# Kernel optimization log

Hardware: AMD Instinct MI355X
Metric: run time of the kernel (lower is better)

## Reference

```python
import jax, jax.numpy as jnp
import numpy as np

N_NODES = 50000
N_EDGES = 800000
NODE_DIM = 256
HIDDEN_DIM = 256
LN_EPS = 1e-5


def setup_inputs() -> dict:
    key = jax.random.key(0)
    ks = jax.random.split(key, 8)
    d, h = NODE_DIM, HIDDEN_DIM
    return {
        "node_features": jax.random.normal(ks[0], (N_NODES, d), jnp.float32),
        "src": jax.random.randint(ks[1], (N_EDGES,), 0, N_NODES, jnp.int32),
        "dst": jax.random.randint(ks[2], (N_EDGES,), 0, N_NODES, jnp.int32),
        "edge_weight": jax.random.uniform(ks[3], (N_EDGES,), jnp.float32),
        "W1": jax.random.normal(ks[4], (d, h), jnp.float32) / np.sqrt(d),
        "b1": jnp.zeros((h,), jnp.float32),
        "g1": jnp.ones((h,), jnp.float32),
        "be1": jnp.zeros((h,), jnp.float32),
        "W2": jax.random.normal(ks[5], (h, h), jnp.float32) / np.sqrt(h),
        "b2": jnp.zeros((h,), jnp.float32),
        "g2": jnp.ones((h,), jnp.float32),
        "be2": jnp.zeros((h,), jnp.float32),
        "Wp": jax.random.normal(ks[6], (h, d), jnp.float32) / np.sqrt(h),
        "bp": jnp.zeros((d,), jnp.float32),
    }


def _spmm(src, dst, w, x, n):
    # sparse adj @ x : agg[i] = sum_{edges e with dst=i} w_e * x[src_e]
    return jax.ops.segment_sum(w[:, None] * x[src], dst, num_segments=n)


def _layer_norm(x, g, b):
    mu = jnp.mean(x, -1, keepdims=True)
    var = jnp.mean(jnp.square(x - mu), -1, keepdims=True)
    return (x - mu) * jax.lax.rsqrt(var + LN_EPS) * g + b


def reference(node_features, src, dst, edge_weight, W1, b1, g1, be1, W2, b2, g2, be2, Wp, bp):
    n = node_features.shape[0]
    x = node_features
    for (W, b, g, be) in ((W1, b1, g1, be1), (W2, b2, g2, be2)):
        agg = _spmm(src, dst, edge_weight, x, n)
        h = (x + agg) @ W + b
        x = jax.nn.gelu(_layer_norm(h, g, be), approximate=False)
        # Dropout(0.1) is identity in eval mode
    return x @ Wp + bp
```

## Files before the change

### kernel.cpp

```cpp
#include <hip/hip_runtime.h>
#include <hip/hip_bf16.h>
#include <math.h>

#define N_NODES 50000
#define N_EDGES 800000
#define DIM 256
#define MPAD 50176
#define LN_EPS 1e-5f
#define SCAN_BLOCKS 196

typedef short bf16x8 __attribute__((ext_vector_type(8)));
typedef float f32x16 __attribute__((ext_vector_type(16)));
typedef unsigned short u16;
typedef u16 u16x8 __attribute__((ext_vector_type(8)));

__device__ __forceinline__ u16 f2bf(float f) {
    union { float f; unsigned u; } v; v.f = f;
    unsigned r = (v.u + 0x7FFFu + ((v.u >> 16) & 1u)) >> 16;
    return (u16)r;
}
__device__ __forceinline__ float bf2f(u16 h) {
    union { unsigned u; float f; } v; v.u = ((unsigned)h) << 16;
    return v.f;
}
__device__ __forceinline__ float gelu_f(float x) {
    float z = x * (1.595769122f + 0.0713548162726f * x * x);
    return x * (1.0f / (1.0f + __expf(-z)));
}

__global__ void count_kernel(const int* __restrict__ dst, int* __restrict__ counts) {
    int e = blockIdx.x * 256 + threadIdx.x;
    if (e < N_EDGES) atomicAdd(&counts[dst[e]], 1);
}

__global__ void scan1_kernel(const int* __restrict__ counts, int* __restrict__ offsets,
                             int* __restrict__ bsum) {
    __shared__ int sh[256];
    int t = threadIdx.x;
    int idx = blockIdx.x * 256 + t;
    int v = (idx < N_NODES) ? counts[idx] : 0;
    sh[t] = v;
    __syncthreads();
#pragma unroll
    for (int off = 1; off < 256; off <<= 1) {
        int u = (t >= off) ? sh[t - off] : 0;
        __syncthreads();
        sh[t] += u;
        __syncthreads();
    }
    if (idx < N_NODES) offsets[idx] = sh[t] - v;
    if (t == 255) bsum[blockIdx.x] = sh[255];
}

__global__ void scan2_kernel(const int* __restrict__ bsum, int* __restrict__ bbase) {
    __shared__ int sh[256];
    int t = threadIdx.x;
    int v = (t < SCAN_BLOCKS) ? bsum[t] : 0;
    sh[t] = v;
    __syncthreads();
#pragma unroll
    for (int off = 1; off < 256; off <<= 1) {
        int u = (t >= off) ? sh[t - off] : 0;
        __syncthreads();
        sh[t] += u;
        __syncthreads();
    }
    if (t < SCAN_BLOCKS) bbase[t] = sh[t] - v;
}

__global__ void scan3_kernel(int* __restrict__ offsets, const int* __restrict__ bbase,
                             int* __restrict__ cursor) {
    int idx = blockIdx.x * 256 + threadIdx.x;
    if (idx < N_NODES) {
        int o = offsets[idx] + bbase[blockIdx.x];
        offsets[idx] = o;
        cursor[idx] = o;
    }
    if (idx == 0) offsets[N_NODES] = N_EDGES;
}

__global__ void scatter_kernel(const int* __restrict__ src, const int* __restrict__ dst,
                               const float* __restrict__ w, int* __restrict__ cursor,
                               int2* __restrict__ ep) {
    int e = blockIdx.x * 256 + threadIdx.x;
    if (e < N_EDGES) {
        int d = dst[e];
        int p = atomicAdd(&cursor[d], 1);
        int2 v; v.x = src[e]; v.y = __float_as_int(w[e]);
        ep[p] = v;
    }
}

__global__ void conv_kernel(const float* __restrict__ in, u16* __restrict__ out) {
    int i = blockIdx.x * 256 + threadIdx.x;
    float4 v = ((const float4*)in)[i];
    ushort4 o;
    o.x = f2bf(v.x); o.y = f2bf(v.y); o.z = f2bf(v.z); o.w = f2bf(v.w);
    ((ushort4*)out)[i] = o;
}

__global__ void convw_kernel(const float* __restrict__ W1, const float* __restrict__ W2,
                             const float* __restrict__ Wp, u16* __restrict__ BF) {
    int idx = blockIdx.x * 256 + threadIdx.x;
    int j = idx & 7;
    int lane = (idx >> 3) & 63;
    int kb = (idx >> 9) & 15;
    int t = (idx >> 13) & 7;
    int m = idx >> 16;
    int n = t * 32 + (lane & 31);
    int k = kb * 16 + (lane >> 5) * 8 + j;
    const float* W = (m == 0) ? W1 : (m == 1) ? W2 : Wp;
    BF[idx] = f2bf(W[k * 256 + n]);
}

__global__ __launch_bounds__(256) void spmm_kernel(
        const u16* __restrict__ x, const int* __restrict__ offs,
        const int2* __restrict__ ep, u16* __restrict__ y) {
    __shared__ u16 tile[32 * 264];
    int tid = threadIdx.x;
    int wave = tid >> 6;
    int lane = tid & 63;
    int node0 = blockIdx.x * 32 + wave * 8;

    const ushort4* xv = (const ushort4*)x;
#pragma unroll 1
    for (int i = 0; i < 8; ++i) {
        int node = node0 + i;
        float a0 = 0, a1 = 0, a2 = 0, a3 = 0;
        float b0 = 0, b1 = 0, b2 = 0, b3 = 0;
        float c0 = 0, c1 = 0, c2 = 0, c3 = 0;
        float d0 = 0, d1 = 0, d2 = 0, d3 = 0;
        if (node < N_NODES) {
            ushort4 v = xv[(size_t)node * 64 + lane];
            a0 = bf2f(v.x); a1 = bf2f(v.y); a2 = bf2f(v.z); a3 = bf2f(v.w);
            int p = offs[node];
            int p1 = offs[node + 1];
            for (; p + 4 <= p1; p += 4) {
                int2 e0 = ep[p],     e1 = ep[p + 1];
                int2 e2 = ep[p + 2], e3 = ep[p + 3];
                int s0 = e0.x; float w0 = __int_as_float(e0.y);
                int s1 = e1.x; float w1 = __int_as_float(e1.y);
                int s2 = e2.x; float w2 = __int_as_float(e2.y);
                int s3 = e3.x; float w3 = __int_as_float(e3.y);
                ushort4 v0 = xv[(size_t)s0 * 64 + lane];
                ushort4 v1 = xv[(size_t)s1 * 64 + lane];
                ushort4 v2 = xv[(size_t)s2 * 64 + lane];
                ushort4 v3 = xv[(size_t)s3 * 64 + lane];
                a0 += w0 * bf2f(v0.x); a1 += w0 * bf2f(v0.y); a2 += w0 * bf2f(v0.z); a3 += w0 * bf2f(v0.w);
                b0 += w1 * bf2f(v1.x); b1 += w1 * bf2f(v1.y); b2 += w1 * bf2f(v1.z); b3 += w1 * bf2f(v1.w);
                c0 += w2 * bf2f(v2.x); c1 += w2 * bf2f(v2.y); c2 += w2 * bf2f(v2.z); c3 += w2 * bf2f(v2.w);
                d0 += w3 * bf2f(v3.x); d1 += w3 * bf2f(v3.y); d2 += w3 * bf2f(v3.z); d3 += w3 * bf2f(v3.w);
            }
            for (; p < p1; ++p) {
                int2 e = ep[p];
                int s = e.x;
                float w = __int_as_float(e.y);
                ushort4 vv = xv[(size_t)s * 64 + lane];
                a0 += w * bf2f(vv.x); a1 += w * bf2f(vv.y); a2 += w * bf2f(vv.z); a3 += w * bf2f(vv.w);
            }
            a0 += b0 + c0 + d0; a1 += b1 + c1 + d1;
            a2 += b2 + c2 + d2; a3 += b3 + c3 + d3;
        }
        ushort4 o;
        o.x = f2bf(a0); o.y = f2bf(a1); o.z = f2bf(a2); o.w = f2bf(a3);
        ((ushort4*)&tile[(wave * 8 + i) * 264])[lane] = o;
    }
    __syncthreads();
    u16* outb = y + (size_t)blockIdx.x * 8192;
#pragma unroll
    for (int hh = 0; hh < 4; ++hh) {
        int gi = tid + hh * 256;
        int kb = gi >> 6;
        int rem = gi & 63;
        int hf = rem >> 5, m = rem & 31;
        u16x8 v = *(const u16x8*)&tile[m * 264 + kb * 16 + hf * 8];
        *(u16x8*)(outb + (size_t)gi * 8) = v;
    }
}

template <int MODE, int OUT_TILED>
__global__ __launch_bounds__(256, 2) void gemm_kernel(
        const u16* __restrict__ A, const u16* __restrict__ BF,
        const float* __restrict__ bias, const float* __restrict__ g,
        const float* __restrict__ be, u16* __restrict__ xb_out,
        float* __restrict__ f_out) {
    int tid = threadIdx.x;
    int wave = tid >> 6, lane = tid & 63;
    int l31 = lane & 31, half = lane >> 5;

    int tile = blockIdx.x * 4 + wave;
    const u16* ga = A + (size_t)tile * 8192 + lane * 8;
    const u16* gb = BF + lane * 8;
    bf16x8 p = *(const bf16x8*)ga;

    f32x16 acc[8];
#pragma unroll
    for (int t = 0; t < 8; ++t)
#pragma unroll
        for (int r = 0; r < 16; ++r) acc[t][r] = 0.f;

#pragma unroll
    for (int kb = 0; kb < 16; ++kb) {
        bf16x8 a = p;
        if (kb < 15) p = *(const bf16x8*)(ga + (kb + 1) * 512);
#pragma unroll
        for (int t = 0; t < 8; ++t) {
            bf16x8 bf = *(const bf16x8*)(gb + (size_t)(t * 16 + kb) * 512);
            acc[t] = __builtin_amdgcn_mfma_f32_32x32x16_bf16(a, bf, acc[t], 0, 0, 0);
        }
    }

    float bv[8];
#pragma unroll
    for (int t = 0; t < 8; ++t) bv[t] = bias[t * 32 + l31];

    if (MODE == 0) {
        float gv[8], bev[8];
#pragma unroll
        for (int t = 0; t < 8; ++t) {
            int c = t * 32 + l31;
            gv[t] = g[c]; bev[t] = be[c];
        }
#pragma unroll
        for (int r = 0; r < 16; ++r) {
            float s = 0.f, q = 0.f;
#pragma unroll
            for (int t = 0; t < 8; ++t) {
                float v = acc[t][r] + bv[t];
                acc[t][r] = v;
                s += v; q += v * v;
            }
            for (int off = 1; off < 32; off <<= 1) {
                s += __shfl_xor(s, off);
                q += __shfl_xor(q, off);
            }
            float mu = s * (1.0f / 256.0f);
            float var = q * (1.0f / 256.0f) - mu * mu;
            float rs = rsqrtf(var + LN_EPS);
            int m = (r & 3) + 8 * (r >> 2) + 4 * half;
            int row = tile * 32 + m;
#pragma unroll
            for (int t = 0; t < 8; ++t) {
                int c = t * 32 + l31;
                float v = (acc[t][r] - mu) * rs * gv[t] + bev[t];
                u16 ob = f2bf(gelu_f(v));
                if (OUT_TILED) {
                    size_t o = (size_t)tile * 8192 +
                               ((size_t)(c >> 4) * 64 + ((c >> 3) & 1) * 32 + m) * 8 + (c & 7);
                    xb_out[o] = ob;
                } else {
                    xb_out[(size_t)row * 256 + c] = ob;
                }
            }
        }
    } else {
#pragma unroll
        for (int r = 0; r < 16; ++r) {
            int m = (r & 3) + 8 * (r >> 2) + 4 * half;
            int row = tile * 32 + m;
            if (row < N_NODES) {
#pragma unroll
                for (int t = 0; t < 8; ++t) {
                    int c = t * 32 + l31;
                    f_out[(size_t)row * 256 + c] = acc[t][r] + bv[t];
                }
            }
        }
    }
}

extern "C" void kernel_launch(void* const* d_in, const int* in_sizes, int n_in,
                              void* d_out, int out_size, void* d_ws, size_t ws_size,
                              hipStream_t stream) {
    const float* nodef = (const float*)d_in[0];
    const int*   src   = (const int*)d_in[1];
    const int*   dst   = (const int*)d_in[2];
    const float* ew    = (const float*)d_in[3];
    const float* W1 = (const float*)d_in[4];
    const float* b1 = (const float*)d_in[5];
    const float* g1 = (const float*)d_in[6];
    const float* be1 = (const float*)d_in[7];
    const float* W2 = (const float*)d_in[8];
    const float* b2 = (const float*)d_in[9];
    const float* g2 = (const float*)d_in[10];
    const float* be2 = (const float*)d_in[11];
    const float* Wp = (const float*)d_in[12];
    const float* bp = (const float*)d_in[13];
    float* out = (float*)d_out;

    char* ws = (char*)d_ws;
    size_t off = 0;
    auto alloc = [&](size_t bytes) -> void* {
        void* p = ws + off;
        off += (bytes + 255) & ~(size_t)255;
        return p;
    };
    u16*   ybuf    = (u16*)alloc((size_t)MPAD * 256 * 2);
    u16*   xbuf    = (u16*)alloc((size_t)MPAD * 256 * 2);
    u16*   WT      = (u16*)alloc((size_t)3 * 65536 * 2);
    int*   counts  = (int*)alloc((size_t)N_NODES * 4);
    int*   offsets = (int*)alloc((size_t)(N_NODES + 1) * 4);
    int*   cursor  = (int*)alloc((size_t)N_NODES * 4);
    int2*  ep      = (int2*)alloc((size_t)N_EDGES * 8);
    int*   bsum    = (int*)alloc((size_t)SCAN_BLOCKS * 4);
    int*   bbase   = (int*)alloc((size_t)SCAN_BLOCKS * 4);

    hipMemsetAsync(counts, 0, (size_t)N_NODES * 4, stream);
    count_kernel<<<(N_EDGES + 255) / 256, 256, 0, stream>>>(dst, counts);
    scan1_kernel<<<SCAN_BLOCKS, 256, 0, stream>>>(counts, offsets, bsum);
    scan2_kernel<<<1, 256, 0, stream>>>(bsum, bbase);
    scan3_kernel<<<SCAN_BLOCKS, 256, 0, stream>>>(offsets, bbase, cursor);
    scatter_kernel<<<(N_EDGES + 255) / 256, 256, 0, stream>>>(src, dst, ew, cursor, ep);
    conv_kernel<<<N_NODES * 64 / 256, 256, 0, stream>>>(nodef, xbuf);
    convw_kernel<<<768, 256, 0, stream>>>(W1, W2, Wp, WT);

    const int GB = MPAD / 128;
    const int SB = MPAD / 32;
    spmm_kernel<<<SB, 256, 0, stream>>>(xbuf, offsets, ep, ybuf);
    gemm_kernel<0, 0><<<GB, 256, 0, stream>>>(ybuf, WT, b1, g1, be1, xbuf, nullptr);
    spmm_kernel<<<SB, 256, 0, stream>>>(xbuf, offsets, ep, ybuf);
    gemm_kernel<0, 1><<<GB, 256, 0, stream>>>(ybuf, WT + 65536, b2, g2, be2, ybuf, nullptr);
    gemm_kernel<1, 0><<<GB, 256, 0, stream>>>(ybuf, WT + 2 * 65536, bp, nullptr, nullptr, nullptr, out);
}
```

Baseline: 443.0 us.

## Fuse SpMM aggregation with GEMM, LayerNorm and GELU per layer

Merges each layer's SpMM kernel and the following GEMM+LayerNorm+GELU kernel into one kernel. The aggregated 32-row tile stays in shared memory and feeds MFMA directly, and each wave computes two 32-column output tiles. LayerNorm statistics are reduced across waves through shared memory. This removes the global write and re-read of the intermediate bf16 tile and two kernel launches. In exchange, every block re-reads the full weight matrix from global/L2 and adds block-wide syncs.

```diff
diff --git a/kernel.cpp b/kernel.cpp
--- a/kernel.cpp
+++ b/kernel.cpp
@@ -113,13 +113,19 @@
     BF[idx] = f2bf(W[k * 256 + n]);
 }
 
-__global__ __launch_bounds__(256) void spmm_kernel(
+template <int OUT_TILED>
+__global__ __launch_bounds__(256, 4) void fused_kernel(
         const u16* __restrict__ x, const int* __restrict__ offs,
-        const int2* __restrict__ ep, u16* __restrict__ y) {
+        const int2* __restrict__ ep, const u16* __restrict__ BF,
+        const float* __restrict__ bias, const float* __restrict__ g,
+        const float* __restrict__ be, u16* __restrict__ out) {
     __shared__ u16 tile[32 * 264];
+    __shared__ float red[32][8];
+    __shared__ float mur[32], rsr[32];
     int tid = threadIdx.x;
     int wave = tid >> 6;
     int lane = tid & 63;
+    int l31 = lane & 31, half = lane >> 5;
     int node0 = blockIdx.x * 32 + wave * 8;
 
     const ushort4* xv = (const ushort4*)x;
@@ -166,31 +172,81 @@
         ((ushort4*)&tile[(wave * 8 + i) * 264])[lane] = o;
     }
     __syncthreads();
-    u16* outb = y + (size_t)blockIdx.x * 8192;
-#pragma unroll
-    for (int hh = 0; hh < 4; ++hh) {
-        int gi = tid + hh * 256;
-        int kb = gi >> 6;
-        int rem = gi & 63;
-        int hf = rem >> 5, m = rem & 31;
-        u16x8 v = *(const u16x8*)&tile[m * 264 + kb * 16 + hf * 8];
-        *(u16x8*)(outb + (size_t)gi * 8) = v;
-    }
-}
-
-template <int MODE, int OUT_TILED>
-__global__ __launch_bounds__(256, 2) void gemm_kernel(
+
+    int t0 = wave * 2, t1 = wave * 2 + 1;
+    const u16* gb = BF + (size_t)lane * 8;
+    f32x16 acc0, acc1;
+#pragma unroll
+    for (int r = 0; r < 16; ++r) { acc0[r] = 0.f; acc1[r] = 0.f; }
+#pragma unroll
+    for (int kb = 0; kb < 16; ++kb) {
+        bf16x8 a = *(const bf16x8*)&tile[l31 * 264 + kb * 16 + half * 8];
+        bf16x8 bf0 = *(const bf16x8*)(gb + (size_t)(t0 * 16 + kb) * 512);
+        bf16x8 bf1 = *(const bf16x8*)(gb + (size_t)(t1 * 16 + kb) * 512);
+        acc0 = __builtin_amdgcn_mfma_f32_32x32x16_bf16(a, bf0, acc0, 0, 0, 0);
+        acc1 = __builtin_amdgcn_mfma_f32_32x32x16_bf16(a, bf1, acc1, 0, 0, 0);
+    }
+
+    float bv0 = bias[t0 * 32 + l31], bv1 = bias[t1 * 32 + l31];
+    float gv0 = g[t0 * 32 + l31],    gv1 = g[t1 * 32 + l31];
+    float ev0 = be[t0 * 32 + l31],   ev1 = be[t1 * 32 + l31];
+#pragma unroll
+    for (int r = 0; r < 16; ++r) {
+        float v0 = acc0[r] + bv0, v1 = acc1[r] + bv1;
+        acc0[r] = v0; acc1[r] = v1;
+        float s = v0 + v1, q = v0 * v0 + v1 * v1;
+#pragma unroll
+        for (int off = 1; off < 32; off <<= 1) {
+            s += __shfl_xor(s, off);
+            q += __shfl_xor(q, off);
+        }
+        if (l31 == 0) {
+            int rw = (r & 3) + 8 * (r >> 2) + 4 * half;
+            red[rw][wave * 2] = s;
+            red[rw][wave * 2 + 1] = q;
+        }
+    }
+    __syncthreads();
+    if (tid < 32) {
+        float s = red[tid][0] + red[tid][2] + red[tid][4] + red[tid][6];
+        float q = red[tid][1] + red[tid][3] + red[tid][5] + red[tid][7];
+        float mu = s * (1.0f / 256.0f);
+        float var = q * (1.0f / 256.0f) - mu * mu;
+        mur[tid] = mu;
+        rsr[tid] = rsqrtf(var + LN_EPS);
+    }
+    __syncthreads();
+#pragma unroll
+    for (int r = 0; r < 16; ++r) {
+        int rw = (r & 3) + 8 * (r >> 2) + 4 * half;
+        float mu = mur[rw], rs = rsr[rw];
+        float v0 = (acc0[r] - mu) * rs * gv0 + ev0;
+        float v1 = (acc1[r] - mu) * rs * gv1 + ev1;
+        u16 o0 = f2bf(gelu_f(v0));
+        u16 o1 = f2bf(gelu_f(v1));
+        int c0 = t0 * 32 + l31, c1 = t1 * 32 + l31;
+        if (OUT_TILED) {
+            size_t base = (size_t)blockIdx.x * 8192;
+            out[base + ((size_t)(c0 >> 4) * 64 + ((c0 >> 3) & 1) * 32 + rw) * 8 + (c0 & 7)] = o0;
+            out[base + ((size_t)(c1 >> 4) * 64 + ((c1 >> 3) & 1) * 32 + rw) * 8 + (c1 & 7)] = o1;
+        } else {
+            size_t rg = (size_t)(blockIdx.x * 32 + rw) * 256;
+            out[rg + c0] = o0;
+            out[rg + c1] = o1;
+        }
+    }
+}
+
+__global__ __launch_bounds__(256, 2) void proj_kernel(
         const u16* __restrict__ A, const u16* __restrict__ BF,
-        const float* __restrict__ bias, const float* __restrict__ g,
-        const float* __restrict__ be, u16* __restrict__ xb_out,
-        float* __restrict__ f_out) {
+        const float* __restrict__ bias, float* __restrict__ f_out) {
     int tid = threadIdx.x;
     int wave = tid >> 6, lane = tid & 63;
     int l31 = lane & 31, half = lane >> 5;
 
     int tile = blockIdx.x * 4 + wave;
     const u16* ga = A + (size_t)tile * 8192 + lane * 8;
-    const u16* gb = BF + lane * 8;
+    const u16* gb = BF + (size_t)lane * 8;
     bf16x8 p = *(const bf16x8*)ga;
 
     f32x16 acc[8];
@@ -214,56 +270,15 @@
 #pragma unroll
     for (int t = 0; t < 8; ++t) bv[t] = bias[t * 32 + l31];
 
-    if (MODE == 0) {
-        float gv[8], bev[8];
-#pragma unroll
-        for (int t = 0; t < 8; ++t) {
-            int c = t * 32 + l31;
-            gv[t] = g[c]; bev[t] = be[c];
-        }
-#pragma unroll
-        for (int r = 0; r < 16; ++r) {
-            float s = 0.f, q = 0.f;
-#pragma unroll
-            for (int t = 0; t < 8; ++t) {
-                float v = acc[t][r] + bv[t];
-                acc[t][r] = v;
-                s += v; q += v * v;
-            }
-            for (int off = 1; off < 32; off <<= 1) {
-                s += __shfl_xor(s, off);
-                q += __shfl_xor(q, off);
-            }
-            float mu = s * (1.0f / 256.0f);
-            float var = q * (1.0f / 256.0f) - mu * mu;
-            float rs = rsqrtf(var + LN_EPS);
-            int m = (r & 3) + 8 * (r >> 2) + 4 * half;
-            int row = tile * 32 + m;
+#pragma unroll
+    for (int r = 0; r < 16; ++r) {
+        int m = (r & 3) + 8 * (r >> 2) + 4 * half;
+        int row = tile * 32 + m;
+        if (row < N_NODES) {
 #pragma unroll
             for (int t = 0; t < 8; ++t) {
                 int c = t * 32 + l31;
-                float v = (acc[t][r] - mu) * rs * gv[t] + bev[t];
-                u16 ob = f2bf(gelu_f(v));
-                if (OUT_TILED) {
-                    size_t o = (size_t)tile * 8192 +
-                               ((size_t)(c >> 4) * 64 + ((c >> 3) & 1) * 32 + m) * 8 + (c & 7);
-                    xb_out[o] = ob;
-                } else {
-                    xb_out[(size_t)row * 256 + c] = ob;
-                }
-            }
-        }
-    } else {
-#pragma unroll
-        for (int r = 0; r < 16; ++r) {
-            int m = (r & 3) + 8 * (r >> 2) + 4 * half;
-            int row = tile * 32 + m;
-            if (row < N_NODES) {
-#pragma unroll
-                for (int t = 0; t < 8; ++t) {
-                    int c = t * 32 + l31;
-                    f_out[(size_t)row * 256 + c] = acc[t][r] + bv[t];
-                }
+                f_out[(size_t)row * 256 + c] = acc[t][r] + bv[t];
             }
         }
     }
@@ -314,11 +329,9 @@
     conv_kernel<<<N_NODES * 64 / 256, 256, 0, stream>>>(nodef, xbuf);
     convw_kernel<<<768, 256, 0, stream>>>(W1, W2, Wp, WT);
 
+    const int SB = MPAD / 32;
     const int GB = MPAD / 128;
-    const int SB = MPAD / 32;
-    spmm_kernel<<<SB, 256, 0, stream>>>(xbuf, offsets, ep, ybuf);
-    gemm_kernel<0, 0><<<GB, 256, 0, stream>>>(ybuf, WT, b1, g1, be1, xbuf, nullptr);
-    spmm_kernel<<<SB, 256, 0, stream>>>(xbuf, offsets, ep, ybuf);
-    gemm_kernel<0, 1><<<GB, 256, 0, stream>>>(ybuf, WT + 65536, b2, g2, be2, ybuf, nullptr);
-    gemm_kernel<1, 0><<<GB, 256, 0, stream>>>(ybuf, WT + 2 * 65536, bp, nullptr, nullptr, nullptr, out);
-}
+    fused_kernel<0><<<SB, 256, 0, stream>>>(xbuf, offsets, ep, WT, b1, g1, be1, ybuf);
+    fused_kernel<1><<<SB, 256, 0, stream>>>(ybuf, offsets, ep, WT + 65536, b2, g2, be2, xbuf);
+    proj_kernel<<<GB, 256, 0, stream>>>(xbuf, WT + 2 * 65536, bp, out);
+}
```

New measurement: 438.3 us. Within noise of the previous version (-1.1%).

## Split SpMM gather into column slices with edge-parallel lane groups

Applied to the files above, without the earlier changes.

Replaces the SpMM kernel with a column-sliced gather. Each block handles one 32-column slice of a 32-node tile, so the grid grows eightfold. Within a wave, four 16-lane groups work on different edges in parallel and are combined with cross-lane shuffles. Each slice also writes straight into the GEMM's tiled layout. The intent is to shrink the per-node gathered row footprint so it fits in cache better and to raise parallelism; the cost is 64-byte row segments per gather, re-reading the edge list once per slice, and more blocks. It also changes which buffer the second GEMM writes and the third GEMM reads.

```diff
diff --git a/kernel.cpp b/kernel.cpp
--- a/kernel.cpp
+++ b/kernel.cpp
@@ -13,6 +13,7 @@
 typedef float f32x16 __attribute__((ext_vector_type(16)));
 typedef unsigned short u16;
 typedef u16 u16x8 __attribute__((ext_vector_type(8)));
+typedef unsigned int u32;
 
 __device__ __forceinline__ u16 f2bf(float f) {
     union { float f; unsigned u; } v; v.f = f;
@@ -113,69 +114,51 @@
     BF[idx] = f2bf(W[k * 256 + n]);
 }
 
-__global__ __launch_bounds__(256) void spmm_kernel(
+__global__ __launch_bounds__(256) void cgather_kernel(
         const u16* __restrict__ x, const int* __restrict__ offs,
         const int2* __restrict__ ep, u16* __restrict__ y) {
-    __shared__ u16 tile[32 * 264];
+    __shared__ __align__(16) u16 stg[1024];
+    int bid = blockIdx.x;
+    int slice = bid & 7;
+    int tile = bid >> 3;
     int tid = threadIdx.x;
-    int wave = tid >> 6;
-    int lane = tid & 63;
-    int node0 = blockIdx.x * 32 + wave * 8;
-
-    const ushort4* xv = (const ushort4*)x;
+    int wave = tid >> 6, lane = tid & 63;
+    int grp = lane >> 4;
+    int l16 = lane & 15;
+    const u16* xs = x + slice * 32;
+
 #pragma unroll 1
     for (int i = 0; i < 8; ++i) {
-        int node = node0 + i;
-        float a0 = 0, a1 = 0, a2 = 0, a3 = 0;
-        float b0 = 0, b1 = 0, b2 = 0, b3 = 0;
-        float c0 = 0, c1 = 0, c2 = 0, c3 = 0;
-        float d0 = 0, d1 = 0, d2 = 0, d3 = 0;
+        int node = tile * 32 + wave * 8 + i;
+        float a0 = 0.f, a1 = 0.f;
         if (node < N_NODES) {
-            ushort4 v = xv[(size_t)node * 64 + lane];
-            a0 = bf2f(v.x); a1 = bf2f(v.y); a2 = bf2f(v.z); a3 = bf2f(v.w);
-            int p = offs[node];
+            if (grp == 0) {
+                u32 sv = *(const u32*)(xs + (size_t)node * 256 + l16 * 2);
+                a0 = __uint_as_float(sv << 16);
+                a1 = __uint_as_float(sv & 0xffff0000u);
+            }
             int p1 = offs[node + 1];
-            for (; p + 4 <= p1; p += 4) {
-                int2 e0 = ep[p],     e1 = ep[p + 1];
-                int2 e2 = ep[p + 2], e3 = ep[p + 3];
-                int s0 = e0.x; float w0 = __int_as_float(e0.y);
-                int s1 = e1.x; float w1 = __int_as_float(e1.y);
-                int s2 = e2.x; float w2 = __int_as_float(e2.y);
-                int s3 = e3.x; float w3 = __int_as_float(e3.y);
-                ushort4 v0 = xv[(size_t)s0 * 64 + lane];
-                ushort4 v1 = xv[(size_t)s1 * 64 + lane];
-                ushort4 v2 = xv[(size_t)s2 * 64 + lane];
-                ushort4 v3 = xv[(size_t)s3 * 64 + lane];
-                a0 += w0 * bf2f(v0.x); a1 += w0 * bf2f(v0.y); a2 += w0 * bf2f(v0.z); a3 += w0 * bf2f(v0.w);
-                b0 += w1 * bf2f(v1.x); b1 += w1 * bf2f(v1.y); b2 += w1 * bf2f(v1.z); b3 += w1 * bf2f(v1.w);
-                c0 += w2 * bf2f(v2.x); c1 += w2 * bf2f(v2.y); c2 += w2 * bf2f(v2.z); c3 += w2 * bf2f(v2.w);
-                d0 += w3 * bf2f(v3.x); d1 += w3 * bf2f(v3.y); d2 += w3 * bf2f(v3.z); d3 += w3 * bf2f(v3.w);
-            }
-            for (; p < p1; ++p) {
+#pragma unroll 1
+            for (int p = offs[node] + grp; p < p1; p += 4) {
                 int2 e = ep[p];
-                int s = e.x;
                 float w = __int_as_float(e.y);
-                ushort4 vv = xv[(size_t)s * 64 + lane];
-                a0 += w * bf2f(vv.x); a1 += w * bf2f(vv.y); a2 += w * bf2f(vv.z); a3 += w * bf2f(vv.w);
-            }
-            a0 += b0 + c0 + d0; a1 += b1 + c1 + d1;
-            a2 += b2 + c2 + d2; a3 += b3 + c3 + d3;
-        }
-        ushort4 o;
-        o.x = f2bf(a0); o.y = f2bf(a1); o.z = f2bf(a2); o.w = f2bf(a3);
-        ((ushort4*)&tile[(wave * 8 + i) * 264])[lane] = o;
+                u32 v = *(const u32*)(xs + (size_t)e.x * 256 + l16 * 2);
+                a0 += w * __uint_as_float(v << 16);
+                a1 += w * __uint_as_float(v & 0xffff0000u);
+            }
+        }
+        a0 += __shfl_xor(a0, 16); a0 += __shfl_xor(a0, 32);
+        a1 += __shfl_xor(a1, 16); a1 += __shfl_xor(a1, 32);
+        if (grp == 0) {
+            int m = wave * 8 + i;
+            int c = l16 * 2;
+            int gidx = (((c >> 4) * 64) + (((c >> 3) & 1) * 32) + m) * 8 + (c & 7);
+            ((u32*)stg)[gidx >> 1] = (u32)f2bf(a0) | ((u32)f2bf(a1) << 16);
+        }
     }
     __syncthreads();
-    u16* outb = y + (size_t)blockIdx.x * 8192;
-#pragma unroll
-    for (int hh = 0; hh < 4; ++hh) {
-        int gi = tid + hh * 256;
-        int kb = gi >> 6;
-        int rem = gi & 63;
-        int hf = rem >> 5, m = rem & 31;
-        u16x8 v = *(const u16x8*)&tile[m * 264 + kb * 16 + hf * 8];
-        *(u16x8*)(outb + (size_t)gi * 8) = v;
-    }
+    uint2* d2 = (uint2*)(y + (size_t)tile * 8192 + (size_t)slice * 1024);
+    d2[tid] = ((const uint2*)stg)[tid];
 }
 
 template <int MODE, int OUT_TILED>
@@ -190,7 +173,7 @@
 
     int tile = blockIdx.x * 4 + wave;
     const u16* ga = A + (size_t)tile * 8192 + lane * 8;
-    const u16* gb = BF + lane * 8;
+    const u16* gb = BF + (size_t)lane * 8;
     bf16x8 p = *(const bf16x8*)ga;
 
     f32x16 acc[8];
@@ -314,11 +297,11 @@
     conv_kernel<<<N_NODES * 64 / 256, 256, 0, stream>>>(nodef, xbuf);
     convw_kernel<<<768, 256, 0, stream>>>(W1, W2, Wp, WT);
 
+    const int CG = (MPAD / 32) * 8;
     const int GB = MPAD / 128;
-    const int SB = MPAD / 32;
-    spmm_kernel<<<SB, 256, 0, stream>>>(xbuf, offsets, ep, ybuf);
+    cgather_kernel<<<CG, 256, 0, stream>>>(xbuf, offsets, ep, ybuf);
     gemm_kernel<0, 0><<<GB, 256, 0, stream>>>(ybuf, WT, b1, g1, be1, xbuf, nullptr);
-    spmm_kernel<<<SB, 256, 0, stream>>>(xbuf, offsets, ep, ybuf);
-    gemm_kernel<0, 1><<<GB, 256, 0, stream>>>(ybuf, WT + 65536, b2, g2, be2, ybuf, nullptr);
-    gemm_kernel<1, 0><<<GB, 256, 0, stream>>>(ybuf, WT + 2 * 65536, bp, nullptr, nullptr, nullptr, out);
-}
+    cgather_kernel<<<CG, 256, 0, stream>>>(xbuf, offsets, ep, ybuf);
+    gemm_kernel<0, 1><<<GB, 256, 0, stream>>>(ybuf, WT + 65536, b2, g2, be2, xbuf, nullptr);
+    gemm_kernel<1, 0><<<GB, 256, 0, stream>>>(xbuf, WT + 2 * 65536, bp, nullptr, nullptr, nullptr, out);
+}
```

Measured after the change: 715.3 us. +61.5%, slower.
